# Kernel optimization log

Measured on AMD Instinct MI355X. Metric: run time of the kernel, lower is better.

Reference implementation:

```python
import jax, jax.numpy as jnp
import numpy as np

TARGET = 8000  # __out_target
B, C, F = 16, 256, 16000


def setup_inputs() -> dict:
    key = jax.random.key(0)
    k1, k2 = jax.random.split(key)
    fe = jax.random.normal(k1, (B, C, F), dtype=jnp.float32)
    # face -> collapse-group assignment produced by the sequential edge-collapse;
    # here randomized but in-range [0, TARGET)
    group_ids = jax.random.randint(k2, (B, F), 0, TARGET, dtype=jnp.int64)
    return {"fe": fe, "group_ids": group_ids}


def reference(fe, group_ids):
    # MeshUnion.rebuild_features: pooled feature = mean of member-face features.
    # fe: [B, C, F] float, group_ids: [B, F] int in [0, TARGET)
    def pool_one(fe_m, gid):  # fe_m: [C, F], gid: [F]
        sums = jax.ops.segment_sum(fe_m.T, gid, num_segments=TARGET)  # [TARGET, C]
        cnt = jax.ops.segment_sum(jnp.ones(gid.shape, fe_m.dtype), gid,
                                  num_segments=TARGET)                # [TARGET]
        return (sums / jnp.maximum(cnt, 1.0)[:, None]).T              # [C, TARGET]

    return jax.vmap(pool_one)(fe, group_ids)  # [B, C, TARGET]
```

## Files before the change

kernel.cpp:

```cpp
#include <hip/hip_runtime.h>
#include <stdint.h>


#define NB 16
#define NC 256
#define NF 16000
#define NT 8000
#define CPB 16

typedef unsigned int uint;
typedef unsigned short ushort;
typedef float f32x4 __attribute__((ext_vector_type(4)));

__device__ __forceinline__ float bf2f(uint h) { return __uint_as_float(h << 16); }
__device__ __forceinline__ uint cvtpk(float lo, float hi) {
    uint r;
    asm("v_cvt_pk_bf16_f32 %0, %1, %2" : "=v"(r) : "v"(lo), "v"(hi));
    return r;
}

__global__ __launch_bounds__(256) void hist_kernel(const int* __restrict__ gid,
                                                   int* __restrict__ cnt) {
    int i = blockIdx.x * 256 + threadIdx.x;
    if (i >= NB * NF / 4) return;
    int4 g = ((const int4*)gid)[i];
    int* c = cnt + (i / (NF / 4)) * NT;
    atomicAdd(&c[g.x], 1);
    atomicAdd(&c[g.y], 1);
    atomicAdd(&c[g.z], 1);
    atomicAdd(&c[g.w], 1);
}

__global__ __launch_bounds__(256) void scanperm_kernel(const int* __restrict__ gid,
                                                       const int* __restrict__ cnt_g,
                                                       uint* __restrict__ zc_g,
                                                       uint* __restrict__ pk,
                                                       ushort* __restrict__ sp) {
    __shared__ int off_s[NT];
    __shared__ int partial[256];
    const int blk = blockIdx.x;
    const int b = blk >> 4, q = blk & 15;
    const int tid = threadIdx.x;
    const int* cnt = cnt_g + b * NT;

    int loc[32], nv[32];
    int ts = 0;
    if (tid < 250) {
        const int4* c4 = (const int4*)(cnt + 32 * tid);
#pragma unroll
        for (int j = 0; j < 8; ++j) {
            int4 v = c4[j];
            loc[4 * j + 0] = ts; nv[4 * j + 0] = v.x; ts += v.x;
            loc[4 * j + 1] = ts; nv[4 * j + 1] = v.y; ts += v.y;
            loc[4 * j + 2] = ts; nv[4 * j + 2] = v.z; ts += v.z;
            loc[4 * j + 3] = ts; nv[4 * j + 3] = v.w; ts += v.w;
        }
    }
    partial[tid] = (tid < 250) ? ts : 0;
    __syncthreads();

    if (tid < 64) {
        int s0 = partial[4 * tid], s1 = partial[4 * tid + 1];
        int s2 = partial[4 * tid + 2], s3 = partial[4 * tid + 3];
        int lsum = s0 + s1 + s2 + s3;
        int inc = lsum;
        for (int d = 1; d < 64; d <<= 1) {
            int u = __shfl_up(inc, d);
            if (tid >= d) inc += u;
        }
        int exc = inc - lsum;
        partial[4 * tid + 0] = exc;
        partial[4 * tid + 1] = exc + s0;
        partial[4 * tid + 2] = exc + s0 + s1;
        partial[4 * tid + 3] = exc + s0 + s1 + s2;
    }
    __syncthreads();

    if (tid < 250) {
        int base = partial[tid];
#pragma unroll
        for (int j = 0; j < 32; ++j) off_s[32 * tid + j] = base + loc[j];
        if (q == 0) {
            uint* pkb = pk + (size_t)b * NT + 32 * tid;
#pragma unroll
            for (int j = 0; j < 32; ++j)
                pkb[j] = (uint)(base + loc[j]) | ((uint)nv[j] << 14);
        }
    }
    __syncthreads();

    if (tid < 250) {
        const int4* g4 = (const int4*)(gid + (size_t)b * NF + q * 1000);
        uint* zc = zc_g + (size_t)b * NT;
        uint2* sp2 = (uint2*)(sp + (size_t)b * NF + q * 1000);
        int4 g = g4[tid];
        uint p0 = (uint)off_s[g.x] + atomicAdd(&zc[g.x], 1u);
        uint p1 = (uint)off_s[g.y] + atomicAdd(&zc[g.y], 1u);
        uint p2 = (uint)off_s[g.z] + atomicAdd(&zc[g.z], 1u);
        uint p3 = (uint)off_s[g.w] + atomicAdd(&zc[g.w], 1u);
        sp2[tid] = make_uint2(p0 | (p1 << 16), p2 | (p3 << 16));
    }
}

#define LGKM_BAR() do {                                          \
        asm volatile("s_waitcnt lgkmcnt(0)" ::: "memory");       \
        __builtin_amdgcn_s_barrier();                            \
        __builtin_amdgcn_sched_barrier(0);                       \
    } while (0)

__global__ __launch_bounds__(1024) void pool_kernel(const float* __restrict__ fe,
                                                    const ushort* __restrict__ sp,
                                                    const uint* __restrict__ pk,
                                                    float* __restrict__ out) {
    extern __shared__ char smem[];
    uint* fes32 = (uint*)smem;
    const int bid = blockIdx.x;
    const int b = bid >> 4, cg = bid & 15;
    const int tid = threadIdx.x;
    const size_t bc0 = (size_t)(b * NC + cg * CPB);
    const bool t3 = (tid < 928);
    const bool t8 = (tid < 832);
    const int tl = t3 ? tid + 3072 : tid;

    const uint2* sp2 = (const uint2*)(sp + (size_t)b * NF);
    uint2 s0 = sp2[tid];
    uint2 s1 = sp2[tid + 1024];
    uint2 s2 = sp2[tid + 2048];
    uint2 s3 = sp2[tl];

    const uint* pkb = pk + (size_t)b * NT;
    uint pv[8];
#pragma unroll
    for (int it = 0; it < 7; ++it) pv[it] = pkb[tid + it * 1024];
    pv[7] = 0;
    if (t8) pv[7] = pkb[7168 + tid];

    const f32x4* fe4base = (const f32x4*)(fe + bc0 * NF);
    f32x4 a0, a1, a2, a3, b0, b1, b2, b3;

    {
        const f32x4* fA = fe4base;
        const f32x4* fB = fe4base + (NF / 4);
        a0 = fA[tid]; a1 = fA[tid + 1024]; a2 = fA[tid + 2048]; a3 = fA[tl];
        b0 = fB[tid]; b1 = fB[tid + 1024]; b2 = fB[tid + 2048]; b3 = fB[tl];
    }

#define PAIR_WRITE(F, S, VA, VB) do {                                    \
        (F)[(S).x & 0xFFFFu] = cvtpk((VA)[0], (VB)[0]);                  \
        (F)[(S).x >> 16]     = cvtpk((VA)[1], (VB)[1]);                  \
        (F)[(S).y & 0xFFFFu] = cvtpk((VA)[2], (VB)[2]);                  \
        (F)[(S).y >> 16]     = cvtpk((VA)[3], (VB)[3]);                  \
    } while (0)

#define GATHER_ST(F, P, T) do {                                          \
        uint p_ = (P);                                                   \
        uint off_ = p_ & 0x3FFFu, n_ = p_ >> 14;                         \
        float sa_ = 0.f, sb_ = 0.f;                                      \
        uint r_ = 0;                                                     \
        for (; r_ + 2 <= n_; r_ += 2) {                                  \
            uint2 w_;                                                    \
            __builtin_memcpy(&w_, &(F)[off_ + r_], 8);                   \
            sa_ += bf2f(w_.x & 0xFFFFu) + bf2f(w_.y & 0xFFFFu);          \
            sb_ += bf2f(w_.x >> 16) + bf2f(w_.y >> 16);                  \
        }                                                                \
        if (r_ < n_) {                                                   \
            uint w_ = (F)[off_ + r_];                                    \
            sa_ += bf2f(w_ & 0xFFFFu);                                   \
            sb_ += bf2f(w_ >> 16);                                       \
        }                                                                \
        float rn_ = n_ ? __builtin_amdgcn_rcpf((float)n_) : 0.f;         \
        __builtin_nontemporal_store(sa_ * rn_, &oA[T]);                  \
        __builtin_nontemporal_store(sb_ * rn_, &oB[T]);                  \
    } while (0)

#pragma unroll
    for (int k = 0; k < CPB / 2; ++k) {
        uint* F = fes32 + (k & 1) * 16000;

        PAIR_WRITE(F, s0, a0, b0);
        PAIR_WRITE(F, s1, a1, b1);
        PAIR_WRITE(F, s2, a2, b2);
        if (t3) PAIR_WRITE(F, s3, a3, b3);

        if (k + 1 < CPB / 2) {
            const f32x4* fA = fe4base + (size_t)(2 * k + 2) * (NF / 4);
            const f32x4* fB = fA + (NF / 4);
            a0 = fA[tid]; a1 = fA[tid + 1024]; a2 = fA[tid + 2048]; a3 = fA[tl];
            b0 = fB[tid]; b1 = fB[tid + 1024]; b2 = fB[tid + 2048]; b3 = fB[tl];
        }

        LGKM_BAR();

        float* oA = out + (bc0 + (size_t)(2 * k)) * NT;
        float* oB = out + (bc0 + (size_t)(2 * k + 1)) * NT;
#pragma unroll
        for (int it = 0; it < 7; ++it) GATHER_ST(F, pv[it], tid + it * 1024);
        if (t8) GATHER_ST(F, pv[7], 7168 + tid);
    }
#undef GATHER_ST
#undef PAIR_WRITE
}

__device__ __forceinline__ void lds_fadd(unsigned addr, float v) {
    asm volatile("ds_add_f32 %0, %1" :: "v"(addr), "v"(v));
}
__global__ __launch_bounds__(256) void pool_fused_kernel(const float* __restrict__ fe,
                                                         const int* __restrict__ gid,
                                                         float* __restrict__ out) {
    __shared__ float acc[NT];
    __shared__ int cnt[NT];
    const int bc = blockIdx.x, b = bc >> 8, tid = threadIdx.x;
    for (int t = tid; t < NT; t += 256) { acc[t] = 0.0f; cnt[t] = 0; }
    __syncthreads();
    const unsigned accb = (unsigned)(uintptr_t)acc;
    const float4* fe4 = (const float4*)(fe + (size_t)bc * NF);
    const int4* gid4 = (const int4*)(gid + (size_t)b * NF);
    for (int i = tid; i < NF / 4; i += 256) {
        float4 v = fe4[i];
        int4 g = gid4[i];
        lds_fadd(accb + 4u * (unsigned)g.x, v.x); atomicAdd(&cnt[g.x], 1);
        lds_fadd(accb + 4u * (unsigned)g.y, v.y); atomicAdd(&cnt[g.y], 1);
        lds_fadd(accb + 4u * (unsigned)g.z, v.z); atomicAdd(&cnt[g.z], 1);
        lds_fadd(accb + 4u * (unsigned)g.w, v.w); atomicAdd(&cnt[g.w], 1);
    }
    asm volatile("s_waitcnt lgkmcnt(0)" ::: "memory");
    __syncthreads();
    float* orow = out + (size_t)bc * NT;
    for (int t = tid; t < NT; t += 256) {
        int n = cnt[t];
        orow[t] = acc[t] / (float)(n > 0 ? n : 1);
    }
}

extern "C" void kernel_launch(void* const* d_in, const int* in_sizes, int n_in,
                              void* d_out, int out_size, void* d_ws, size_t ws_size,
                              hipStream_t stream) {
    const float* fe = (const float*)d_in[0];
    const int* gid = (const int*)d_in[1];
    float* out = (float*)d_out;

    const size_t O_CNT = 0;
    const size_t O_ZC  = 512000;
    const size_t O_PK  = 1024000;
    const size_t O_SP  = 1536000;
    const size_t TOTAL = 2048000;

    if (ws_size >= TOTAL) {
        char* w = (char*)d_ws;
        int* cnt = (int*)(w + O_CNT);
        uint* zc = (uint*)(w + O_ZC);
        uint* pk = (uint*)(w + O_PK);
        ushort* sp = (ushort*)(w + O_SP);

        static bool lds_opted = false;
        if (!lds_opted) {
            (void)hipFuncSetAttribute((const void*)pool_kernel,
                                      hipFuncAttributeMaxDynamicSharedMemorySize,
                                      128000);
            lds_opted = true;
        }

        (void)hipMemsetAsync(w, 0, 1024000, stream);
        hist_kernel<<<(NB * NF / 4 + 255) / 256, 256, 0, stream>>>(gid, cnt);
        scanperm_kernel<<<NB * 16, 256, 0, stream>>>(gid, cnt, zc, pk, sp);
        pool_kernel<<<NB * (NC / CPB), 1024, 128000, stream>>>(fe, sp, pk, out);
    } else {
        pool_fused_kernel<<<NB * NC, 256, 0, stream>>>(fe, gid, out);
    }
}
```

Baseline: 104.7 us.

## Fuse scan and slot computation into pool kernel, record occurrence indices in histogram

The histogram kernel now keeps the atomicAdd return value as each face's occurrence rank within its group and writes it to a workspace array. The separate scan/permutation kernel is removed. Each pool block recomputes the per-batch exclusive scan of group counts in LDS and derives sorted slot positions from gid, occ and the scanned offsets. This drops one kernel launch, the second set of atomics and the zc memset, but every one of the 16 blocks per batch redoes the scan and the slot computation, and the extra block-wide barriers come before the main feature loads.

```diff
diff --git a/kernel.cpp b/kernel.cpp
--- a/kernel.cpp
+++ b/kernel.cpp
@@ -20,86 +20,18 @@
 }
 
 __global__ __launch_bounds__(256) void hist_kernel(const int* __restrict__ gid,
-                                                   int* __restrict__ cnt) {
+                                                   int* __restrict__ cnt,
+                                                   ushort* __restrict__ occ) {
     int i = blockIdx.x * 256 + threadIdx.x;
     if (i >= NB * NF / 4) return;
     int4 g = ((const int4*)gid)[i];
     int* c = cnt + (i / (NF / 4)) * NT;
-    atomicAdd(&c[g.x], 1);
-    atomicAdd(&c[g.y], 1);
-    atomicAdd(&c[g.z], 1);
-    atomicAdd(&c[g.w], 1);
-}
-
-__global__ __launch_bounds__(256) void scanperm_kernel(const int* __restrict__ gid,
-                                                       const int* __restrict__ cnt_g,
-                                                       uint* __restrict__ zc_g,
-                                                       uint* __restrict__ pk,
-                                                       ushort* __restrict__ sp) {
-    __shared__ int off_s[NT];
-    __shared__ int partial[256];
-    const int blk = blockIdx.x;
-    const int b = blk >> 4, q = blk & 15;
-    const int tid = threadIdx.x;
-    const int* cnt = cnt_g + b * NT;
-
-    int loc[32], nv[32];
-    int ts = 0;
-    if (tid < 250) {
-        const int4* c4 = (const int4*)(cnt + 32 * tid);
-#pragma unroll
-        for (int j = 0; j < 8; ++j) {
-            int4 v = c4[j];
-            loc[4 * j + 0] = ts; nv[4 * j + 0] = v.x; ts += v.x;
-            loc[4 * j + 1] = ts; nv[4 * j + 1] = v.y; ts += v.y;
-            loc[4 * j + 2] = ts; nv[4 * j + 2] = v.z; ts += v.z;
-            loc[4 * j + 3] = ts; nv[4 * j + 3] = v.w; ts += v.w;
-        }
-    }
-    partial[tid] = (tid < 250) ? ts : 0;
-    __syncthreads();
-
-    if (tid < 64) {
-        int s0 = partial[4 * tid], s1 = partial[4 * tid + 1];
-        int s2 = partial[4 * tid + 2], s3 = partial[4 * tid + 3];
-        int lsum = s0 + s1 + s2 + s3;
-        int inc = lsum;
-        for (int d = 1; d < 64; d <<= 1) {
-            int u = __shfl_up(inc, d);
-            if (tid >= d) inc += u;
-        }
-        int exc = inc - lsum;
-        partial[4 * tid + 0] = exc;
-        partial[4 * tid + 1] = exc + s0;
-        partial[4 * tid + 2] = exc + s0 + s1;
-        partial[4 * tid + 3] = exc + s0 + s1 + s2;
-    }
-    __syncthreads();
-
-    if (tid < 250) {
-        int base = partial[tid];
-#pragma unroll
-        for (int j = 0; j < 32; ++j) off_s[32 * tid + j] = base + loc[j];
-        if (q == 0) {
-            uint* pkb = pk + (size_t)b * NT + 32 * tid;
-#pragma unroll
-            for (int j = 0; j < 32; ++j)
-                pkb[j] = (uint)(base + loc[j]) | ((uint)nv[j] << 14);
-        }
-    }
-    __syncthreads();
-
-    if (tid < 250) {
-        const int4* g4 = (const int4*)(gid + (size_t)b * NF + q * 1000);
-        uint* zc = zc_g + (size_t)b * NT;
-        uint2* sp2 = (uint2*)(sp + (size_t)b * NF + q * 1000);
-        int4 g = g4[tid];
-        uint p0 = (uint)off_s[g.x] + atomicAdd(&zc[g.x], 1u);
-        uint p1 = (uint)off_s[g.y] + atomicAdd(&zc[g.y], 1u);
-        uint p2 = (uint)off_s[g.z] + atomicAdd(&zc[g.z], 1u);
-        uint p3 = (uint)off_s[g.w] + atomicAdd(&zc[g.w], 1u);
-        sp2[tid] = make_uint2(p0 | (p1 << 16), p2 | (p3 << 16));
-    }
+    uint o0 = (uint)atomicAdd(&c[g.x], 1);
+    uint o1 = (uint)atomicAdd(&c[g.y], 1);
+    uint o2 = (uint)atomicAdd(&c[g.z], 1);
+    uint o3 = (uint)atomicAdd(&c[g.w], 1);
+    ((ushort4*)occ)[i] = make_ushort4((ushort)o0, (ushort)o1,
+                                      (ushort)o2, (ushort)o3);
 }
 
 #define LGKM_BAR() do {                                          \
@@ -109,31 +41,82 @@
     } while (0)
 
 __global__ __launch_bounds__(1024) void pool_kernel(const float* __restrict__ fe,
-                                                    const ushort* __restrict__ sp,
-                                                    const uint* __restrict__ pk,
+                                                    const int* __restrict__ gid,
+                                                    const ushort* __restrict__ occ,
+                                                    const int* __restrict__ cnt,
                                                     float* __restrict__ out) {
     extern __shared__ char smem[];
     uint* fes32 = (uint*)smem;
+    uint* pkl = (uint*)smem;
+    int* wpart = (int*)(smem + 64000);
     const int bid = blockIdx.x;
     const int b = bid >> 4, cg = bid & 15;
     const int tid = threadIdx.x;
+    const int lane = tid & 63, wid = tid >> 6;
     const size_t bc0 = (size_t)(b * NC + cg * CPB);
     const bool t3 = (tid < 928);
     const bool t8 = (tid < 832);
     const int tl = t3 ? tid + 3072 : tid;
 
-    const uint2* sp2 = (const uint2*)(sp + (size_t)b * NF);
-    uint2 s0 = sp2[tid];
-    uint2 s1 = sp2[tid + 1024];
-    uint2 s2 = sp2[tid + 2048];
-    uint2 s3 = sp2[tl];
-
-    const uint* pkb = pk + (size_t)b * NT;
+    int loc[8], nv[8];
+    int ts = 0;
+    if (tid < 1000) {
+        const int4* c4 = (const int4*)(cnt + (size_t)b * NT + 8 * tid);
+        int4 v0 = c4[0], v1 = c4[1];
+        loc[0] = ts; nv[0] = v0.x; ts += v0.x;
+        loc[1] = ts; nv[1] = v0.y; ts += v0.y;
+        loc[2] = ts; nv[2] = v0.z; ts += v0.z;
+        loc[3] = ts; nv[3] = v0.w; ts += v0.w;
+        loc[4] = ts; nv[4] = v1.x; ts += v1.x;
+        loc[5] = ts; nv[5] = v1.y; ts += v1.y;
+        loc[6] = ts; nv[6] = v1.z; ts += v1.z;
+        loc[7] = ts; nv[7] = v1.w; ts += v1.w;
+    }
+    int inc = ts;
+    for (int d = 1; d < 64; d <<= 1) {
+        int u = __shfl_up(inc, d);
+        if (lane >= d) inc += u;
+    }
+    if (lane == 63) wpart[wid] = inc;
+    __syncthreads();
+    {
+        int wbase = 0;
+        for (int wv = 0; wv < wid; ++wv) wbase += wpart[wv];
+        int base = wbase + inc - ts;
+        if (tid < 1000) {
+#pragma unroll
+            for (int j = 0; j < 8; ++j)
+                pkl[8 * tid + j] = (uint)(base + loc[j]) | ((uint)nv[j] << 14);
+        }
+    }
+    __syncthreads();
+
     uint pv[8];
 #pragma unroll
-    for (int it = 0; it < 7; ++it) pv[it] = pkb[tid + it * 1024];
+    for (int it = 0; it < 7; ++it) pv[it] = pkl[tid + it * 1024];
     pv[7] = 0;
-    if (t8) pv[7] = pkb[7168 + tid];
+    if (t8) pv[7] = pkl[7168 + tid];
+
+    uint2 s0, s1, s2, s3;
+    {
+        const int4* g4 = (const int4*)(gid + (size_t)b * NF);
+        const ushort4* o4 = (const ushort4*)(occ + (size_t)b * NF);
+        int4 ga = g4[tid], gb4 = g4[tid + 1024];
+        int4 gc = g4[tid + 2048], gd = g4[tl];
+        ushort4 oa = o4[tid], ob = o4[tid + 1024];
+        ushort4 oc = o4[tid + 2048], od = o4[tl];
+#define SLOT(G, O) ((pkl[(uint)(G)] & 0x3FFFu) + (uint)(O))
+        s0 = make_uint2(SLOT(ga.x, oa.x) | (SLOT(ga.y, oa.y) << 16),
+                        SLOT(ga.z, oa.z) | (SLOT(ga.w, oa.w) << 16));
+        s1 = make_uint2(SLOT(gb4.x, ob.x) | (SLOT(gb4.y, ob.y) << 16),
+                        SLOT(gb4.z, ob.z) | (SLOT(gb4.w, ob.w) << 16));
+        s2 = make_uint2(SLOT(gc.x, oc.x) | (SLOT(gc.y, oc.y) << 16),
+                        SLOT(gc.z, oc.z) | (SLOT(gc.w, oc.w) << 16));
+        s3 = make_uint2(SLOT(gd.x, od.x) | (SLOT(gd.y, od.y) << 16),
+                        SLOT(gd.z, od.z) | (SLOT(gd.w, od.w) << 16));
+#undef SLOT
+    }
+    __syncthreads();
 
     const f32x4* fe4base = (const f32x4*)(fe + bc0 * NF);
     f32x4 a0, a1, a2, a3, b0, b1, b2, b3;
@@ -240,17 +223,13 @@
     float* out = (float*)d_out;
 
     const size_t O_CNT = 0;
-    const size_t O_ZC  = 512000;
-    const size_t O_PK  = 1024000;
-    const size_t O_SP  = 1536000;
-    const size_t TOTAL = 2048000;
+    const size_t O_OCC = 512000;
+    const size_t TOTAL = 1024000;
 
     if (ws_size >= TOTAL) {
         char* w = (char*)d_ws;
         int* cnt = (int*)(w + O_CNT);
-        uint* zc = (uint*)(w + O_ZC);
-        uint* pk = (uint*)(w + O_PK);
-        ushort* sp = (ushort*)(w + O_SP);
+        ushort* occ = (ushort*)(w + O_OCC);
 
         static bool lds_opted = false;
         if (!lds_opted) {
@@ -260,10 +239,9 @@
             lds_opted = true;
         }
 
-        (void)hipMemsetAsync(w, 0, 1024000, stream);
-        hist_kernel<<<(NB * NF / 4 + 255) / 256, 256, 0, stream>>>(gid, cnt);
-        scanperm_kernel<<<NB * 16, 256, 0, stream>>>(gid, cnt, zc, pk, sp);
-        pool_kernel<<<NB * (NC / CPB), 1024, 128000, stream>>>(fe, sp, pk, out);
+        (void)hipMemsetAsync(cnt, 0, 512000, stream);
+        hist_kernel<<<(NB * NF / 4 + 255) / 256, 256, 0, stream>>>(gid, cnt, occ);
+        pool_kernel<<<NB * (NC / CPB), 1024, 128000, stream>>>(fe, gid, occ, cnt, out);
     } else {
         pool_fused_kernel<<<NB * NC, 256, 0, stream>>>(fe, gid, out);
     }
```

After: 94.44 us (median of 2 runs). 1.11x faster.
